# Optimization experiments

Hardware: AMD Instinct MI355X
Metric: run time of the kernel (lower is better)

The kernel has to match this reference:

```python
import jax, jax.numpy as jnp
import numpy as np

B, L, X, Y, A = 32, 1024, 1024, 1024, 16


def setup_inputs() -> dict:
    key = jax.random.key(0)
    ks = jax.random.split(key, 6)
    stdv = 1.0 / np.sqrt(X)
    stdv_h = 1.0 / np.sqrt(Y)
    return {
        "x": jax.random.normal(ks[0], (B, L, X), dtype=jnp.float32),
        "y": jax.random.normal(ks[1], (B, Y), dtype=jnp.float32),
        "x_mask": jnp.zeros((B, L), dtype=bool),
        "actions": jax.random.randint(ks[2], (B,), 0, A),
        "weight": jax.random.uniform(ks[3], (Y, X), minval=-stdv, maxval=stdv, dtype=jnp.float32),
        "bias": jnp.zeros((X,), dtype=jnp.float32),
        "wa_h": jax.random.uniform(ks[4], (A, Y, 1), minval=-stdv_h, maxval=stdv_h, dtype=jnp.float32),
    }


def reference(x, y, x_mask, actions, weight, bias, wa_h):
    # Per-action column scores: softmax over x_size of sum_y(weight * wa_h[a])
    # (equivalent to the torch loop: a2 = weight*wa_h[a]; softmax(a2.sum(0)))
    score2 = jax.nn.softmax(jnp.einsum("yx,ay->ax", weight, wa_h[:, :, 0]), axis=-1)  # [A, X]
    # u[b,a,:] = y[b] @ (weight * score2[a]) = (y@weight)[b] * score2[a];
    # the one-hot mask then selects row actions[b] -> gather instead of A GEMMs.
    yW = y @ weight                                   # [B, X]
    Wy = yW * score2[actions] + bias                  # [B, X]
    xWy = jnp.einsum("blx,bx->bl", x, Wy)             # [B, L]
    xWy = jnp.where(x_mask, -jnp.inf, xWy)
    return jax.nn.log_softmax(xWy, axis=-1)  # training mode
```

## Files before the change

kernel.cpp:

```cpp
#include <hip/hip_runtime.h>
#include <hip/hip_bf16.h>
#include <math.h>

constexpr int Ac = 16;
constexpr int Bc = 32;
constexpr int Lc = 1024;
constexpr int Xc = 1024;
constexpr int Yc = 1024;
constexpr int Cc = Ac + Bc;

__device__ __forceinline__ float waveReduceSum(float v) {
#pragma unroll
    for (int off = 32; off > 0; off >>= 1) v += __shfl_down(v, off, 64);
    return v;
}

__device__ __forceinline__ float waveReduceMax(float v) {
#pragma unroll
    for (int off = 32; off > 0; off >>= 1) v = fmaxf(v, __shfl_down(v, off, 64));
    return v;
}

__global__ __launch_bounds__(256) void k1_proj(
        const float* __restrict__ weight, const float* __restrict__ yv,
        const float* __restrict__ wa_h, float* __restrict__ s_raw,
        float* __restrict__ yW) {
    const int x  = blockIdx.x * 256 + threadIdx.x;
    const int y0 = blockIdx.y * 16;

    __shared__ float cLDS[Cc][16];

#pragma unroll
    for (int k = 0; k < 3; ++k) {
        const int idx = threadIdx.x + k * 256;
        const int row = idx >> 4;
        const int col = idx & 15;
        cLDS[row][col] = (row < Ac) ? wa_h[row * Yc + y0 + col]
                                    : yv[(row - Ac) * Yc + y0 + col];
    }

    float w[16];
#pragma unroll
    for (int t = 0; t < 16; ++t) w[t] = weight[(size_t)(y0 + t) * Xc + x];

    __syncthreads();

    float acc[Cc];
#pragma unroll
    for (int j = 0; j < Cc; ++j) acc[j] = 0.0f;

    const float4* cvec = (const float4*)cLDS;
#pragma unroll
    for (int j = 0; j < Cc; ++j) {
#pragma unroll
        for (int q = 0; q < 4; ++q) {
            const float4 c = cvec[j * 4 + q];
            acc[j] = fmaf(w[q * 4 + 0], c.x, acc[j]);
            acc[j] = fmaf(w[q * 4 + 1], c.y, acc[j]);
            acc[j] = fmaf(w[q * 4 + 2], c.z, acc[j]);
            acc[j] = fmaf(w[q * 4 + 3], c.w, acc[j]);
        }
    }

#pragma unroll
    for (int j = 0; j < Ac; ++j) atomicAdd(&s_raw[j * Xc + x], acc[j]);
#pragma unroll
    for (int j = Ac; j < Cc; ++j) atomicAdd(&yW[(j - Ac) * Xc + x], acc[j]);
}

__global__ __launch_bounds__(256) void k2_softmax(
        const float* __restrict__ s_raw, float* __restrict__ score2) {
    const int a    = blockIdx.x;
    const int tid  = threadIdx.x;
    const int wave = tid >> 6;
    const int lane = tid & 63;
    __shared__ float smax[4];
    __shared__ float ssum[4];

    float v[4];
    float mx = -INFINITY;
#pragma unroll
    for (int k = 0; k < 4; ++k) {
        v[k] = s_raw[a * Xc + tid + k * 256];
        mx = fmaxf(mx, v[k]);
    }
    mx = waveReduceMax(mx);
    if (lane == 0) smax[wave] = mx;
    __syncthreads();
    mx = fmaxf(fmaxf(smax[0], smax[1]), fmaxf(smax[2], smax[3]));

    float sum = 0.0f;
#pragma unroll
    for (int k = 0; k < 4; ++k) {
        v[k] = __expf(v[k] - mx);
        sum += v[k];
    }
    sum = waveReduceSum(sum);
    if (lane == 0) ssum[wave] = sum;
    __syncthreads();
    sum = ssum[0] + ssum[1] + ssum[2] + ssum[3];

    const float inv = 1.0f / sum;
#pragma unroll
    for (int k = 0; k < 4; ++k) score2[a * Xc + tid + k * 256] = v[k] * inv;
}

__global__ __launch_bounds__(256) void k3_dot(
        const float* __restrict__ x, const float* __restrict__ yW,
        const float* __restrict__ score2, const float* __restrict__ bias,
        const int* __restrict__ actions, float* __restrict__ xWy) {
    const int b  = blockIdx.y;
    const int l0 = blockIdx.x * 16;
    __shared__ float Wy[Xc];

    const int act = actions[b];
#pragma unroll
    for (int k = 0; k < 4; ++k) {
        const int xi = threadIdx.x + k * 256;
        Wy[xi] = fmaf(yW[b * Xc + xi], score2[act * Xc + xi], bias[xi]);
    }
    __syncthreads();

    const int wave = threadIdx.x >> 6;
    const int lane = threadIdx.x & 63;
    const float4* WyV = (const float4*)Wy;

    for (int r = wave; r < 16; r += 4) {
        const int l = l0 + r;
        const float4* xp = (const float4*)(x + ((size_t)b * Lc + l) * Xc);
        float acc = 0.0f;
#pragma unroll
        for (int k = 0; k < 4; ++k) {
            const int idx = lane + k * 64;
            const float4 xv = xp[idx];
            const float4 wv = WyV[idx];
            acc = fmaf(xv.x, wv.x, acc);
            acc = fmaf(xv.y, wv.y, acc);
            acc = fmaf(xv.z, wv.z, acc);
            acc = fmaf(xv.w, wv.w, acc);
        }
        acc = waveReduceSum(acc);
        if (lane == 0) xWy[b * Lc + l] = acc;
    }
}

__global__ __launch_bounds__(256) void k4_logsoftmax(
        const float* __restrict__ xWy, const unsigned char* __restrict__ mask,
        float* __restrict__ out) {
    const int b    = blockIdx.x;
    const int tid  = threadIdx.x;
    const int wave = tid >> 6;
    const int lane = tid & 63;
    __shared__ float smax[4];
    __shared__ float ssum[4];

    float v[4];
    float mx = -INFINITY;
#pragma unroll
    for (int k = 0; k < 4; ++k) {
        const int l = tid + k * 256;
        float t = xWy[b * Lc + l];
        if (mask[b * Lc + l]) t = -INFINITY;
        v[k] = t;
        mx = fmaxf(mx, t);
    }
    mx = waveReduceMax(mx);
    if (lane == 0) smax[wave] = mx;
    __syncthreads();
    mx = fmaxf(fmaxf(smax[0], smax[1]), fmaxf(smax[2], smax[3]));

    float sum = 0.0f;
#pragma unroll
    for (int k = 0; k < 4; ++k) sum += __expf(v[k] - mx);
    sum = waveReduceSum(sum);
    if (lane == 0) ssum[wave] = sum;
    __syncthreads();
    sum = ssum[0] + ssum[1] + ssum[2] + ssum[3];

    const float lse = mx + __logf(sum);
#pragma unroll
    for (int k = 0; k < 4; ++k) out[b * Lc + tid + k * 256] = v[k] - lse;
}

extern "C" void kernel_launch(void* const* d_in, const int* in_sizes, int n_in,
                              void* d_out, int out_size, void* d_ws, size_t ws_size,
                              hipStream_t stream) {
    const float* x          = (const float*)d_in[0];
    const float* yv         = (const float*)d_in[1];
    const unsigned char* xm = (const unsigned char*)d_in[2];
    const int* actions      = (const int*)d_in[3];
    const float* weight     = (const float*)d_in[4];
    const float* bias       = (const float*)d_in[5];
    const float* wa_h       = (const float*)d_in[6];
    float* out              = (float*)d_out;

    char* ws      = (char*)d_ws;
    float* s_raw  = (float*)(ws);
    float* yW     = (float*)(ws + 64 * 1024);
    float* score2 = (float*)(ws + 192 * 1024);
    float* xWy    = (float*)(ws + 256 * 1024);

    hipMemsetAsync(d_ws, 0, 192 * 1024, stream);

    k1_proj<<<dim3(Xc / 256, Yc / 16), 256, 0, stream>>>(weight, yv, wa_h, s_raw, yW);
    k2_softmax<<<Ac, 256, 0, stream>>>(s_raw, score2);
    k3_dot<<<dim3(Lc / 16, Bc), 256, 0, stream>>>(x, yW, score2, bias, actions, xWy);
    k4_logsoftmax<<<Bc, 256, 0, stream>>>(xWy, xm, out);
}
```

Before: 223.8 us.

## Replace atomic accumulation with partial-sum buffer reduced in fused softmax/Wy kernel

The projection kernel now writes per-Y-chunk partial sums to a workspace instead of issuing global atomicAdds, which also removes the memset. A new 1024-thread kernel per action reduces the partials, computes the column softmax, and directly builds Wy for the batches that select that action, so the dot kernel only copies a precomputed Wy row. This trades atomic contention and a memset for a 12 MB partial buffer that has to be written and read back, and the Wy stage now runs on only 16 blocks.

```diff
diff --git a/kernel.cpp b/kernel.cpp
--- a/kernel.cpp
+++ b/kernel.cpp
@@ -8,6 +8,7 @@
 constexpr int Xc = 1024;
 constexpr int Yc = 1024;
 constexpr int Cc = Ac + Bc;
+constexpr int NCH = 64;
 
 __device__ __forceinline__ float waveReduceSum(float v) {
 #pragma unroll
@@ -23,8 +24,7 @@
 
 __global__ __launch_bounds__(256) void k1_proj(
         const float* __restrict__ weight, const float* __restrict__ yv,
-        const float* __restrict__ wa_h, float* __restrict__ s_raw,
-        float* __restrict__ yW) {
+        const float* __restrict__ wa_h, float* __restrict__ partial) {
     const int x  = blockIdx.x * 256 + threadIdx.x;
     const int y0 = blockIdx.y * 16;
 
@@ -62,68 +62,67 @@
         }
     }
 
-#pragma unroll
-    for (int j = 0; j < Ac; ++j) atomicAdd(&s_raw[j * Xc + x], acc[j]);
-#pragma unroll
-    for (int j = Ac; j < Cc; ++j) atomicAdd(&yW[(j - Ac) * Xc + x], acc[j]);
-}
-
-__global__ __launch_bounds__(256) void k2_softmax(
-        const float* __restrict__ s_raw, float* __restrict__ score2) {
+    float* dst = partial + ((size_t)blockIdx.y * Cc) * Xc + x;
+#pragma unroll
+    for (int j = 0; j < Cc; ++j) dst[j * Xc] = acc[j];
+}
+
+__global__ __launch_bounds__(1024) void k2_softmax_wy(
+        const float* __restrict__ partial, const float* __restrict__ bias,
+        const int* __restrict__ actions, float* __restrict__ Wy) {
     const int a    = blockIdx.x;
-    const int tid  = threadIdx.x;
-    const int wave = tid >> 6;
-    const int lane = tid & 63;
-    __shared__ float smax[4];
-    __shared__ float ssum[4];
-
-    float v[4];
-    float mx = -INFINITY;
-#pragma unroll
-    for (int k = 0; k < 4; ++k) {
-        v[k] = s_raw[a * Xc + tid + k * 256];
-        mx = fmaxf(mx, v[k]);
-    }
-    mx = waveReduceMax(mx);
+    const int x    = threadIdx.x;
+    const int wave = threadIdx.x >> 6;
+    const int lane = threadIdx.x & 63;
+    __shared__ float smax[16];
+    __shared__ float ssum[16];
+
+    float s = 0.0f;
+#pragma unroll 8
+    for (int yc = 0; yc < NCH; ++yc)
+        s += partial[((size_t)yc * Cc + a) * Xc + x];
+
+    float mx = waveReduceMax(s);
     if (lane == 0) smax[wave] = mx;
     __syncthreads();
-    mx = fmaxf(fmaxf(smax[0], smax[1]), fmaxf(smax[2], smax[3]));
-
-    float sum = 0.0f;
-#pragma unroll
-    for (int k = 0; k < 4; ++k) {
-        v[k] = __expf(v[k] - mx);
-        sum += v[k];
-    }
-    sum = waveReduceSum(sum);
+#pragma unroll
+    for (int i = 0; i < 16; ++i) mx = fmaxf(mx, smax[i]);
+
+    const float e = __expf(s - mx);
+    float sum = waveReduceSum(e);
     if (lane == 0) ssum[wave] = sum;
     __syncthreads();
-    sum = ssum[0] + ssum[1] + ssum[2] + ssum[3];
-
-    const float inv = 1.0f / sum;
-#pragma unroll
-    for (int k = 0; k < 4; ++k) score2[a * Xc + tid + k * 256] = v[k] * inv;
+    sum = 0.0f;
+#pragma unroll
+    for (int i = 0; i < 16; ++i) sum += ssum[i];
+
+    const float p  = e / sum;
+    const float bi = bias[x];
+
+    for (int b = 0; b < Bc; ++b) {
+        if (actions[b] == a) {
+            float acc = 0.0f;
+#pragma unroll 8
+            for (int yc = 0; yc < NCH; ++yc)
+                acc += partial[((size_t)yc * Cc + Ac + b) * Xc + x];
+            Wy[b * Xc + x] = fmaf(acc, p, bi);
+        }
+    }
 }
 
 __global__ __launch_bounds__(256) void k3_dot(
-        const float* __restrict__ x, const float* __restrict__ yW,
-        const float* __restrict__ score2, const float* __restrict__ bias,
-        const int* __restrict__ actions, float* __restrict__ xWy) {
+        const float* __restrict__ x, const float* __restrict__ Wy,
+        float* __restrict__ xWy) {
     const int b  = blockIdx.y;
     const int l0 = blockIdx.x * 16;
-    __shared__ float Wy[Xc];
-
-    const int act = actions[b];
-#pragma unroll
-    for (int k = 0; k < 4; ++k) {
-        const int xi = threadIdx.x + k * 256;
-        Wy[xi] = fmaf(yW[b * Xc + xi], score2[act * Xc + xi], bias[xi]);
-    }
+    __shared__ float WyS[Xc];
+
+    ((float4*)WyS)[threadIdx.x] = ((const float4*)(Wy + (size_t)b * Xc))[threadIdx.x];
     __syncthreads();
 
     const int wave = threadIdx.x >> 6;
     const int lane = threadIdx.x & 63;
-    const float4* WyV = (const float4*)Wy;
+    const float4* WyV = (const float4*)WyS;
 
     for (int r = wave; r < 16; r += 4) {
         const int l = l0 + r;
@@ -194,16 +193,13 @@
     const float* wa_h       = (const float*)d_in[6];
     float* out              = (float*)d_out;
 
-    char* ws      = (char*)d_ws;
-    float* s_raw  = (float*)(ws);
-    float* yW     = (float*)(ws + 64 * 1024);
-    float* score2 = (float*)(ws + 192 * 1024);
-    float* xWy    = (float*)(ws + 256 * 1024);
-
-    hipMemsetAsync(d_ws, 0, 192 * 1024, stream);
-
-    k1_proj<<<dim3(Xc / 256, Yc / 16), 256, 0, stream>>>(weight, yv, wa_h, s_raw, yW);
-    k2_softmax<<<Ac, 256, 0, stream>>>(s_raw, score2);
-    k3_dot<<<dim3(Lc / 16, Bc), 256, 0, stream>>>(x, yW, score2, bias, actions, xWy);
+    char* ws       = (char*)d_ws;
+    float* partial = (float*)(ws);
+    float* Wy      = (float*)(ws + (size_t)NCH * Cc * Xc * 4);
+    float* xWy     = (float*)(ws + (size_t)NCH * Cc * Xc * 4 + 128 * 1024);
+
+    k1_proj<<<dim3(Xc / 256, NCH), 256, 0, stream>>>(weight, yv, wa_h, partial);
+    k2_softmax_wy<<<Ac, 1024, 0, stream>>>(partial, bias, actions, Wy);
+    k3_dot<<<dim3(Lc / 16, Bc), 256, 0, stream>>>(x, Wy, xWy);
     k4_logsoftmax<<<Bc, 256, 0, stream>>>(xWy, xm, out);
 }
```

Result: slower. 238.0 us (+6.4%).
